# Performance work log

Measured on AMD Instinct MI355X. Metric: run time of the kernel, lower is better.

The kernel has to match this reference:

```python
import jax, jax.numpy as jnp
import numpy as np

EPS = 1e-12  # torch F.normalize eps


def unfold(x, ksize, pad):
    # torch F.unfold equivalent: [B,C,H,W] -> [B, C*k*k, L], channel-major ordering
    patches = jax.lax.conv_general_dilated_patches(
        x, (ksize, ksize), (1, 1), [(pad, pad), (pad, pad)],
        dimension_numbers=('NCHW', 'OIHW', 'NCHW'))
    B, CKK, Hp, Wp = patches.shape
    return patches.reshape(B, CKK, Hp * Wp)


def fold(patches, C, ksize, H, W, pad):
    # torch F.fold equivalent (stride 1): overlap-add of [B, C*k*k, H*W] -> [B,C,H,W]
    B = patches.shape[0]
    p = patches.reshape(B, C, ksize, ksize, H, W)
    out = jnp.zeros((B, C, H + 2 * pad, W + 2 * pad), patches.dtype)
    for di in range(ksize):
        for dj in range(ksize):
            out = out.at[:, :, di:di + H, dj:dj + W].add(p[:, :, di, dj])
    return out[:, :, pad:pad + H, pad:pad + W]


def setup_inputs() -> dict:
    key = jax.random.key(0)
    ks = jax.random.split(key, 4)
    B, C, H, W = 2, 512, 64, 64
    D, CIN = 256, 512 * 9  # embed: Linear(tdim*8*3*3 -> tdim*4), tdim=64
    return {
        'query': jax.random.normal(ks[0], (B, C, H, W), dtype=jnp.float32),
        'key': jax.random.normal(ks[1], (B, C, H, W), dtype=jnp.float32),
        'value': jax.random.normal(ks[2], (B, C, H, W), dtype=jnp.float32),
        'W_embed': jax.random.normal(ks[3], (D, CIN), dtype=jnp.float32) * 0.02,
        'k': 3,
    }


def reference(query, key, value, W_embed, k):
    B, Cv, H, W = value.shape
    # patch embed: unfold -> linear (no bias)
    q_unf = unfold(query, k, k // 2)                       # [B, C*k*k, L]
    k_unf = unfold(key, k, k // 2)                         # [B, C*k*k, L]
    k_emb = jnp.einsum('bcl,dc->bld', k_unf, W_embed)      # [B, L, D]
    q_emb = jnp.einsum('bcl,dc->bdl', q_unf, W_embed)      # [B, D, L]
    # cosine correlation
    k_n = k_emb / jnp.maximum(jnp.linalg.norm(k_emb, axis=2, keepdims=True), EPS)
    q_n = q_emb / jnp.maximum(jnp.linalg.norm(q_emb, axis=1, keepdims=True), EPS)
    corr = jnp.einsum('bld,bdm->blm', k_n, q_n)            # [B, L_key, L_query]
    corr_value = jnp.max(corr, axis=1)                     # [B, L]
    corr_argmax = jnp.argmax(corr, axis=1)                 # [B, L]
    # swap(V=value, idx=corr_argmax, s=1, k=k)
    s = 1
    temph = s * k + H * s - H - s                          # = k - 1
    tempw = s * k + W * s - W - s
    ph = max(temph // 2 + temph % 2, 1)
    pw = max(tempw // 2 + tempw % 2, 1)
    v_unf = unfold(value, k, ph)                           # [B, Cv*k*k, L] (ph==pw for square)
    t_unf = jnp.take_along_axis(v_unf, corr_argmax[:, None, :], axis=2)
    divisor = fold(jnp.ones_like(t_unf), Cv, k, H, W, ph)
    T = fold(t_unf, Cv, k, H, W, ph) / divisor             # [B, Cv, H, W]
    S = corr_value.reshape(B, 1, H, W)
    return S, T
```

## Files before the change

### kernel.cpp

```cpp
#include <hip/hip_runtime.h>
#include <hip/hip_bf16.h>
#include <stdint.h>
#include <math.h>

#define BB 2
#define CC 512
#define HH 64
#define WW 64
#define LL 4096
#define DD 256
#define CIN 4608
#define NG 144

typedef _Float16 half_t;
typedef __attribute__((ext_vector_type(8))) _Float16 f16x8;
typedef __attribute__((ext_vector_type(4))) _Float16 f16x4;
typedef __attribute__((ext_vector_type(4))) float f32x4;

__global__ __launch_bounds__(256) void presplit(const float* __restrict__ query,
                                                const float* __restrict__ key,
                                                char* __restrict__ img_ts) {
    __shared__ float tile[32][65];
    int img = blockIdx.y;
    int y   = blockIdx.x;
    const float* src = ((img >> 1) ? key : query) + (size_t)(img & 1) * CC * LL + y * WW;
    char* dstbase = img_ts + ((size_t)img * 64 + y) * (16 * 64 * 128);
    int t = threadIdx.x;
    int xl = t & 63, c4 = t >> 6;
    int xw = t >> 2, fsw = t & 3;
    for (int cc = 0; cc < 16; ++cc) {
#pragma unroll
        for (int j = 0; j < 8; ++j) {
            int cl = c4 + j * 4;
            tile[cl][xl] = src[(size_t)(cc * 32 + cl) * LL + xl];
        }
        __syncthreads();
        f16x8 h8, l8;
#pragma unroll
        for (int j = 0; j < 8; ++j) {
            float v = tile[fsw * 8 + j][xw];
            half_t h = (half_t)v;
            h8[j] = h; l8[j] = (half_t)(v - (float)h);
        }
        char* p = dstbase + (size_t)cc * 8192 + xw * 128;
        int swz = (xw & 7) << 4;
        *(f16x8*)(p + ((fsw * 16) ^ swz)) = h8;
        *(f16x8*)(p + ((64 + fsw * 16) ^ swz)) = l8;
        __syncthreads();
    }
}

__global__ __launch_bounds__(256) void splitW2b(const float* __restrict__ W,
                                                char* __restrict__ Wst) {
    int i = blockIdx.x * 256 + threadIdx.x;
    if (i >= NG * DD * 4) return;
    int g  = i >> 10;
    int r  = i & 1023;
    int d  = r >> 2;
    int fs = r & 3;
    int cc = g / 9, o = g - cc * 9;
    const float* src = W + (size_t)d * CIN;
    f16x8 h8, l8;
#pragma unroll
    for (int j = 0; j < 8; j++) {
        float w = src[(cc * 32 + fs * 8 + j) * 9 + o];
        half_t h = (half_t)w;
        h8[j] = h;
        l8[j] = (half_t)(w - (float)h);
    }
    size_t base = (size_t)g * 32768 + d * 128;
    int sw = (d & 7) << 4;
    *(f16x8*)(Wst + base + ((fs * 16) ^ sw)) = h8;
    *(f16x8*)(Wst + base + ((64 + fs * 16) ^ sw)) = l8;
}

#define GATE() do { asm volatile("s_waitcnt vmcnt(0) lgkmcnt(0)" ::: "memory"); \
                    __builtin_amdgcn_s_barrier(); \
                    __builtin_amdgcn_sched_barrier(0); } while (0)

__global__ __launch_bounds__(512, 1) void embed_mfma(const char* __restrict__ img_ts,
                                                     const char* __restrict__ Wst,
                                                     const char* __restrict__ zp,
                                                     float* __restrict__ part) {
    __shared__ char sW[2][32768];
    __shared__ char sB[2][33792];

    int iid = blockIdx.y;
    int ks  = blockIdx.z;
    int lt  = blockIdx.x;
    int y0  = lt * 2;
    int t = threadIdx.x;
    int w = t >> 6, lane = t & 63;
    int wr = w >> 1, wc = w & 1;
    int fr = lane & 15, fs = lane >> 4;

    const char* imgb = img_ts + (size_t)iid * (64 * 16 * 64 * 128) + (size_t)ks * 65536;
    const char *ps0, *ps1, *ps2, *ps3, *ps4;
    int pb0, pb1, pb2, pb3, pb4;
#define PREP(qv, PS, PB)                                                \
    {                                                                   \
        int q = (qv);                                                   \
        int ri = q / 528;                                               \
        int rem = q - ri * 528;                                         \
        int xi = rem >> 3, sub = rem & 7;                               \
        int xg = xi - 1, yg = y0 - 1 + ri;                              \
        bool ok = (yg >= 0) && (yg < 64) && (xg >= 0) && (xg < 64);     \
        PS = ok ? imgb + (size_t)yg * 131072 + (size_t)xg * 128 + sub * 16 \
                : zp + ((q & 255) * 16);                                \
        PB = ok ? 8192 : 0;                                             \
    }
    PREP(t, ps0, pb0); PREP(512 + t, ps1, pb1); PREP(1024 + t, ps2, pb2);
    PREP(1536 + t, ps3, pb3); PREP(2048 + t, ps4, pb4);

    const char* pW = Wst + (size_t)ks * 72 * 32768;

#define GLL(src, dst)                                                   \
    __builtin_amdgcn_global_load_lds(                                   \
        (const __attribute__((address_space(1))) void*)(src),           \
        (__attribute__((address_space(3))) void*)(dst), 16, 0, 0)

#define DMAW(dst)                                                       \
    do {                                                                \
        _Pragma("unroll")                                               \
        for (int c = 0; c < 4; c++)                                     \
            GLL(pW + c * 8192 + t * 16, (dst) + c * 8192 + t * 16);     \
        pW += 32768;                                                    \
    } while (0)

#define DMAB(dst)                                                       \
    do {                                                                \
        GLL(ps0, (dst) + t * 16);                                       \
        GLL(ps1, (dst) + 8192 + t * 16);                                \
        GLL(ps2, (dst) + 16384 + t * 16);                               \
        GLL(ps3, (dst) + 24576 + t * 16);                               \
        if (t < 64) GLL(ps4, (dst) + 32768 + t * 16);                   \
        ps0 += pb0; ps1 += pb1; ps2 += pb2; ps3 += pb3; ps4 += pb4;     \
    } while (0)

#define READA(wbuf)                                                     \
    do {                                                                \
        _Pragma("unroll")                                               \
        for (int rg = 0; rg < 4; rg++) {                                \
            int dl = wr * 64 + rg * 16 + fr;                            \
            int sw_ = (dl & 7) << 4;                                    \
            const char* rowp = (const char*)(wbuf) + dl * 128;          \
            ah[rg] = *(const f16x8*)(rowp + ((fs * 16) ^ sw_));         \
            al[rg] = *(const f16x8*)(rowp + ((64 + fs * 16) ^ sw_));    \
        }                                                               \
    } while (0)

#define READB(bbuf, di_, dj_)                                           \
    do {                                                                \
        int ri = wc + (di_);                                            \
        _Pragma("unroll")                                               \
        for (int cg = 0; cg < 4; cg++) {                                \
            int xi = cg * 16 + fr + (dj_);                              \
            int sw_ = ((xi - 1) & 7) << 4;                              \
            const char* rowp = (const char*)(bbuf) + ri * 8448 + xi * 128; \
            bh[cg] = *(const f16x8*)(rowp + ((fs * 16) ^ sw_));         \
            bl[cg] = *(const f16x8*)(rowp + ((64 + fs * 16) ^ sw_));    \
        }                                                               \
    } while (0)

#define DOMFMA()                                                        \
    do {                                                                \
        _Pragma("unroll")                                               \
        for (int rg = 0; rg < 4; rg++)                                  \
            _Pragma("unroll")                                           \
            for (int cg = 0; cg < 4; cg++)                              \
                acc[rg][cg] = __builtin_amdgcn_mfma_f32_16x16x32_f16(ah[rg], bh[cg], acc[rg][cg], 0, 0, 0); \
        _Pragma("unroll")                                               \
        for (int rg = 0; rg < 4; rg++)                                  \
            _Pragma("unroll")                                           \
            for (int cg = 0; cg < 4; cg++) {                            \
                acc[rg][cg] = __builtin_amdgcn_mfma_f32_16x16x32_f16(ah[rg], bl[cg], acc[rg][cg], 0, 0, 0); \
                acc[rg][cg] = __builtin_amdgcn_mfma_f32_16x16x32_f16(al[rg], bh[cg], acc[rg][cg], 0, 0, 0); \
            }                                                           \
    } while (0)

    f32x4 acc[4][4];
#pragma unroll
    for (int rg = 0; rg < 4; rg++)
#pragma unroll
        for (int cg = 0; cg < 4; cg++) acc[rg][cg] = (f32x4){0.f, 0.f, 0.f, 0.f};

    f16x8 ah[4], al[4], bh[4], bl[4];

    char* wb0 = &sW[0][0]; char* wb1 = &sW[1][0];
    char* b0 = &sB[0][0];  char* b1 = &sB[1][0];

    DMAB(b0);
    DMAW(wb0);
    GATE();

    char* wcur = wb0; char* wnext = wb1;
    char* bcur = b0;  char* bnext = b1;
    int o = 0, ccl = 0;

#pragma unroll 1
    for (int g = 0; g < 72; ++g) {
        int di_ = (o >= 6) ? 2 : (o >= 3) ? 1 : 0;
        int dj_ = o - di_ * 3;
        READA(wcur);
        READB(bcur, di_, dj_);
        if (g < 71) DMAW(wnext);
        if (o == 8 && ccl < 7) DMAB(bnext);
        __builtin_amdgcn_sched_barrier(0);
        DOMFMA();
        GATE();
        { char* tp = wcur; wcur = wnext; wnext = tp; }
        if (o == 8) { char* tp = bcur; bcur = bnext; bnext = tp; o = 0; ccl++; }
        else o++;
    }

    float* pt = part + (((size_t)iid * 32 + lt) * 2 + ks) * 32768;
#pragma unroll
    for (int rg = 0; rg < 4; rg++)
#pragma unroll
        for (int cg = 0; cg < 4; cg++) {
            int l = wc * 64 + cg * 16 + fr;
            int d0 = wr * 64 + rg * 16 + fs * 4;
#pragma unroll
            for (int r = 0; r < 4; r++)
                pt[(d0 + r) * 128 + l] = acc[rg][cg][r];
        }
#undef PREP
#undef GLL
#undef DMAW
#undef DMAB
#undef READA
#undef READB
#undef DOMFMA
}

__global__ __launch_bounds__(256) void norm_split(const float* __restrict__ part,
                                                  char* __restrict__ qemb,
                                                  char* __restrict__ kemb) {
    __shared__ float sm[4][64];
    __shared__ float invn[64];
    __shared__ char stage[64][1040];

    int iid = blockIdx.y;
    int bx  = blockIdx.x;
    int lt  = bx >> 1, lh2 = bx & 1;
    const float* p0 = part + (((size_t)iid * 32 + lt) * 2 + 0) * 32768 + lh2 * 64;
    const float* p1 = p0 + 32768;
    int t = threadIdx.x;
    int ll = t & 63, dq = t >> 6;

    float sq = 0.f;
    for (int dd = 0; dd < 64; ++dd) {
        int d = dq * 64 + dd;
        float v = p0[d * 128 + ll] + p1[d * 128 + ll];
        sq += v * v;
    }
    sm[dq][ll] = sq;
    __syncthreads();
    if (t < 64) {
        float s = sm[0][t] + sm[1][t] + sm[2][t] + sm[3][t];
        invn[t] = 1.0f / fmaxf(sqrtf(s), 1e-12f);
    }
    __syncthreads();

    float sc = invn[ll];
    int swb = (ll & 7) << 4;
    for (int oc = 0; oc < 8; ++oc) {
        int d0 = dq * 64 + oc * 8;
        f16x8 h8, l8;
#pragma unroll
        for (int j = 0; j < 8; ++j) {
            int d = d0 + j;
            float v = (p0[d * 128 + ll] + p1[d * 128 + ll]) * sc;
            half_t h = (half_t)v;
            h8[j] = h;
            l8[j] = (half_t)(v - (float)h);
        }
        int itb = d0 >> 5;
        int fsc = (d0 >> 3) & 3;
        *(f16x8*)&stage[ll][itb * 128 + ((fsc * 16) ^ swb)] = h8;
        *(f16x8*)&stage[ll][itb * 128 + ((64 + fsc * 16) ^ swb)] = l8;
    }
    __syncthreads();

    int b = iid & 1, type = iid >> 1;
    char* e = (type ? kemb : qemb);
    int rr = t >> 2, c0 = t & 3;
    char* erow = e + ((size_t)b * LL + lt * 128 + lh2 * 64 + rr) * 1024;
    const char* srow = &stage[rr][0];
#pragma unroll
    for (int c = 0; c < 16; ++c) {
        int cj = c0 + c * 4;
        *(float4*)(erow + cj * 16) = *(const float4*)(srow + cj * 16);
    }
}

__global__ void init_packed(unsigned long long* p, int n) {
    int i = blockIdx.x * 256 + threadIdx.x;
    if (i < n) p[i] = 0ull;
}

__global__ __launch_bounds__(256, 2) void corr_max_mfma(const char* __restrict__ kemb,
                                                        const char* __restrict__ qemb,
                                                        unsigned long long* __restrict__ packed) {
    __shared__ char sA[2][16384];
    __shared__ char sBq[2][16384];

    int b  = blockIdx.z;
    int l0 = blockIdx.y * 128;
    int m0 = blockIdx.x * 128;
    int t  = threadIdx.x;
    int w = t >> 6, lane = t & 63;
    int wr = w >> 1, wc = w & 1;
    int fr = lane & 15, fs = lane >> 4;

    const char* Abase = kemb + ((size_t)b * LL + l0) * 1024;
    const char* Bbase = qemb + ((size_t)b * LL + m0) * 1024;

    f32x4 acc[4][4];
#pragma unroll
    for (int i = 0; i < 4; i++)
#pragma unroll
        for (int j = 0; j < 4; j++) acc[i][j] = (f32x4){0.f, 0.f, 0.f, 0.f};

#define DMA2(bufi, itv)                                                   \
    do {                                                                  \
        _Pragma("unroll")                                                 \
        for (int c = 0; c < 4; c++) {                                     \
            int idx = c * 4096 + t * 16;                                  \
            int row = idx >> 7, offb = idx & 127;                         \
            __builtin_amdgcn_global_load_lds(                             \
                (const __attribute__((address_space(1))) void*)(Abase + (size_t)row * 1024 + (itv) * 128 + offb), \
                (__attribute__((address_space(3))) void*)(&sA[bufi][idx]), 16, 0, 0); \
        }                                                                 \
        _Pragma("unroll")                                                 \
        for (int c = 0; c < 4; c++) {                                     \
            int idx = c * 4096 + t * 16;                                  \
            int row = idx >> 7, offb = idx & 127;                         \
            __builtin_amdgcn_global_load_lds(                             \
                (const __attribute__((address_space(1))) void*)(Bbase + (size_t)row * 1024 + (itv) * 128 + offb), \
                (__attribute__((address_space(3))) void*)(&sBq[bufi][idx]), 16, 0, 0); \
        }                                                                 \
    } while (0)

    DMA2(0, 0);

    f16x8 ah[4], al[4], bh[4], bl[4];
    for (int it = 0; it < 8; ++it) {
        asm volatile("s_waitcnt vmcnt(0) lgkmcnt(0)" ::: "memory");
        __builtin_amdgcn_s_barrier();
        __builtin_amdgcn_sched_barrier(0);
        if (it < 7) DMA2((it + 1) & 1, it + 1);
        __builtin_amdgcn_sched_barrier(0);
        const char* sa = sA[it & 1];
        const char* sb = sBq[it & 1];
#pragma unroll
        for (int rg = 0; rg < 4; rg++) {
            int r = wr * 64 + rg * 16 + fr;
            const char* rp = sa + r * 128;
            int sw_ = (r & 7) << 4;
            ah[rg] = *(const f16x8*)(rp + ((fs * 16) ^ sw_));
            al[rg] = *(const f16x8*)(rp + ((64 + fs * 16) ^ sw_));
        }
#pragma unroll
        for (int cg = 0; cg < 4; cg++) {
            int r = wc * 64 + cg * 16 + fr;
            const char* rp = sb + r * 128;
            int sw_ = (r & 7) << 4;
            bh[cg] = *(const f16x8*)(rp + ((fs * 16) ^ sw_));
            bl[cg] = *(const f16x8*)(rp + ((64 + fs * 16) ^ sw_));
        }
#pragma unroll
        for (int rg = 0; rg < 4; rg++)
#pragma unroll
            for (int cg = 0; cg < 4; cg++)
                acc[rg][cg] = __builtin_amdgcn_mfma_f32_16x16x32_f16(ah[rg], bh[cg], acc[rg][cg], 0, 0, 0);
#pragma unroll
        for (int rg = 0; rg < 4; rg++)
#pragma unroll
            for (int cg = 0; cg < 4; cg++) {
                acc[rg][cg] = __builtin_amdgcn_mfma_f32_16x16x32_f16(ah[rg], bl[cg], acc[rg][cg], 0, 0, 0);
                acc[rg][cg] = __builtin_amdgcn_mfma_f32_16x16x32_f16(al[rg], bh[cg], acc[rg][cg], 0, 0, 0);
            }
    }
#undef DMA2

#pragma unroll
    for (int cg = 0; cg < 4; cg++) {
        unsigned long long best = 0ull;
#pragma unroll
        for (int rg = 0; rg < 4; rg++) {
#pragma unroll
            for (int r = 0; r < 4; r++) {
                unsigned u = __float_as_uint(acc[rg][cg][r]);
                u = (u & 0x80000000u) ? ~u : (u | 0x80000000u);
                int l = l0 + wr * 64 + rg * 16 + fs * 4 + r;
                unsigned long long p = ((unsigned long long)u << 32) | (unsigned)(4095 - l);
                best = (p > best) ? p : best;
            }
        }
        unsigned long long oo;
        oo = __shfl_xor(best, 16); best = (oo > best) ? oo : best;
        oo = __shfl_xor(best, 32); best = (oo > best) ? oo : best;
        if (lane < 16)
            atomicMax(&packed[(size_t)b * LL + m0 + wc * 64 + cg * 16 + lane], best);
    }
}

__global__ void decode_packed(const unsigned long long* __restrict__ packed,
                              float* __restrict__ S_out, int* __restrict__ arg) {
    int i = blockIdx.x * 256 + threadIdx.x;
    if (i < BB * LL) {
        unsigned long long p = packed[i];
        unsigned u = (unsigned)(p >> 32);
        unsigned bits = (u & 0x80000000u) ? (u & 0x7FFFFFFFu) : ~u;
        S_out[i] = __uint_as_float(bits);
        arg[i] = 4095 - (int)(unsigned)(p & 0xFFFFFFFFull);
    }
}

__global__ __launch_bounds__(256) void transpose_mat(const float* __restrict__ src,
                                                     float* __restrict__ dst,
                                                     int R, int Cc) {
    __shared__ float tile[32][33];
    size_t boff = (size_t)blockIdx.z * R * Cc;
    int bx = blockIdx.x;
    int by = blockIdx.y;
    int tx = threadIdx.x & 31;
    int ty = threadIdx.x >> 5;
    const float* s = src + boff;
    float* d = dst + boff;
#pragma unroll
    for (int i = 0; i < 4; i++) {
        int r = by * 32 + ty + i * 8;
        int c = bx * 32 + tx;
        tile[ty + i * 8][tx] = s[(size_t)r * Cc + c];
    }
    __syncthreads();
#pragma unroll
    for (int i = 0; i < 4; i++) {
        int c = bx * 32 + ty + i * 8;
        int r = by * 32 + tx;
        d[(size_t)c * R + r] = tile[tx][ty + i * 8];
    }
}

__global__ __launch_bounds__(256) void gather_fold(const float* __restrict__ value_t,
                                                   const int* __restrict__ arg,
                                                   float* __restrict__ T_t) {
    int b = blockIdx.y;
    int pix = blockIdx.x;
    int y = pix >> 6, x = pix & 63;
    int t = threadIdx.x;
    float2 acc = make_float2(0.f, 0.f);
    int cnty = (y == 0 || y == HH - 1) ? 2 : 3;
    int cntx = (x == 0 || x == WW - 1) ? 2 : 3;
    const int* ab = arg + b * LL;
    const float* vb = value_t + (size_t)b * LL * CC;
#pragma unroll
    for (int di = 0; di < 3; di++) {
        int my = y + 1 - di;
        if (my < 0 || my >= HH) continue;
#pragma unroll
        for (int dj = 0; dj < 3; dj++) {
            int mx = x + 1 - dj;
            if (mx < 0 || mx >= WW) continue;
            int a = ab[my * WW + mx];
            int ay = a >> 6, ax = a & 63;
            int vy = ay + di - 1, vx = ax + dj - 1;
            if (vy < 0 || vy >= HH || vx < 0 || vx >= WW) continue;
            float2 v = *(const float2*)&vb[((size_t)(vy * WW + vx)) * CC + t * 2];
            acc.x += v.x; acc.y += v.y;
        }
    }
    float inv = 1.0f / (float)(cnty * cntx);
    acc.x *= inv; acc.y *= inv;
    *(float2*)&T_t[((size_t)b * LL + pix) * CC + t * 2] = acc;
}

extern "C" void kernel_launch(void* const* d_in, const int* in_sizes, int n_in,
                              void* d_out, int out_size, void* d_ws, size_t ws_size,
                              hipStream_t stream) {
    const float* query = (const float*)d_in[0];
    const float* key   = (const float*)d_in[1];
    const float* value = (const float*)d_in[2];
    const float* Wemb  = (const float*)d_in[3];

    float* out   = (float*)d_out;
    float* S_out = out;
    float* T_out = out + BB * LL;

    char* ws = (char*)d_ws;
    char*  img_ts = ws;
    char*  Wst    = ws + 33554432;
    float* part   = (float*)(ws + 38273024);
    char*  qemb   = ws + 71827456;
    char*  kemb   = ws + 80216064;
    unsigned long long* packed = (unsigned long long*)(ws + 88604672);
    char*  zp     = ws + 88670208;
    int*   arg    = (int*)(ws + 88674304);
    float* val_t  = (float*)(ws + 38273024);
    float* T_t    = (float*)(ws + 38273024 + 16777216);

    init_packed   <<<dim3(34), 256, 0, stream>>>(packed, 8704);
    presplit      <<<dim3(64, 4), 256, 0, stream>>>(query, key, img_ts);
    splitW2b      <<<dim3(576), 256, 0, stream>>>(Wemb, Wst);
    embed_mfma    <<<dim3(32, 4, 2), 512, 0, stream>>>(img_ts, Wst, zp, part);
    norm_split    <<<dim3(64, 4), 256, 0, stream>>>(part, qemb, kemb);
    corr_max_mfma <<<dim3(32, 32, 2), 256, 0, stream>>>(kemb, qemb, packed);
    decode_packed <<<dim3(32), 256, 0, stream>>>(packed, S_out, arg);
    transpose_mat <<<dim3(128, 16, 2), 256, 0, stream>>>(value, val_t, CC, LL);
    gather_fold   <<<dim3(4096, 2), 256, 0, stream>>>(val_t, arg, T_t);
    transpose_mat <<<dim3(16, 128, 2), 256, 0, stream>>>(T_t, T_out, LL, CC);
}
```

Baseline: 221.7 us.

## Restructure embed GEMM pipeline with unrolled double-buffered A loads and 8x1 wave tiling

Reworks the embed MFMA kernel. Each wave now owns 32 output rows across all 128 columns instead of a 4x2 wave grid. The 72-step loop is fully unrolled into 18-step bodies with precomputed LDS pointers, and weight fragments for the next step are prefetched into alternating register sets. The wait-all plus barrier gate is replaced with partial vmcnt waits and a barrier only at image-tile boundaries, so global loads overlap compute. Launch bounds request two blocks per CU, which limits registers, and norm_split caches values in registers so the partial-sum buffer is not read twice. Fewer barriers raise the risk of LDS race conditions if the vmcnt accounting is wrong.

```diff
diff --git a/kernel.cpp b/kernel.cpp
--- a/kernel.cpp
+++ b/kernel.cpp
@@ -74,11 +74,7 @@
     *(f16x8*)(Wst + base + ((64 + fs * 16) ^ sw)) = l8;
 }
 
-#define GATE() do { asm volatile("s_waitcnt vmcnt(0) lgkmcnt(0)" ::: "memory"); \
-                    __builtin_amdgcn_s_barrier(); \
-                    __builtin_amdgcn_sched_barrier(0); } while (0)
-
-__global__ __launch_bounds__(512, 1) void embed_mfma(const char* __restrict__ img_ts,
+__global__ __launch_bounds__(512, 2) void embed_mfma(const char* __restrict__ img_ts,
                                                      const char* __restrict__ Wst,
                                                      const char* __restrict__ zp,
                                                      float* __restrict__ part) {
@@ -91,7 +87,6 @@
     int y0  = lt * 2;
     int t = threadIdx.x;
     int w = t >> 6, lane = t & 63;
-    int wr = w >> 1, wc = w & 1;
     int fr = lane & 15, fs = lane >> 4;
 
     const char* imgb = img_ts + (size_t)iid * (64 * 16 * 64 * 128) + (size_t)ks * 65536;
@@ -112,114 +107,137 @@
     PREP(t, ps0, pb0); PREP(512 + t, ps1, pb1); PREP(1024 + t, ps2, pb2);
     PREP(1536 + t, ps3, pb3); PREP(2048 + t, ps4, pb4);
 
-    const char* pW = Wst + (size_t)ks * 72 * 32768;
+    const char* pWl = Wst + (size_t)ks * 72 * 32768 + (w << 12) + lane * 16;
+    char* wdst0 = &sW[0][0] + (w << 12) + lane * 16;
+    char* wdst1 = wdst0 + 32768;
+    char* bB0 = &sB[0][0] + t * 16;
+
+    int swzA = (fr & 7) << 4;
+    const char* aBH = &sW[0][0] + (w << 12) + fr * 128 + ((fs * 16) ^ swzA);
+    const char* aBL = &sW[0][0] + (w << 12) + fr * 128 + ((64 + fs * 16) ^ swzA);
+    const char* bH0 = &sB[0][0] + (fr + 0) * 128 + ((fs * 16) ^ (((fr - 1) & 7) << 4));
+    const char* bL0 = &sB[0][0] + (fr + 0) * 128 + (((64 + fs * 16)) ^ (((fr - 1) & 7) << 4));
+    const char* bH1 = &sB[0][0] + (fr + 1) * 128 + ((fs * 16) ^ (((fr) & 7) << 4));
+    const char* bL1 = &sB[0][0] + (fr + 1) * 128 + (((64 + fs * 16)) ^ (((fr) & 7) << 4));
+    const char* bH2 = &sB[0][0] + (fr + 2) * 128 + ((fs * 16) ^ (((fr + 1) & 7) << 4));
+    const char* bL2 = &sB[0][0] + (fr + 2) * 128 + (((64 + fs * 16)) ^ (((fr + 1) & 7) << 4));
 
 #define GLL(src, dst)                                                   \
     __builtin_amdgcn_global_load_lds(                                   \
         (const __attribute__((address_space(1))) void*)(src),           \
         (__attribute__((address_space(3))) void*)(dst), 16, 0, 0)
 
-#define DMAW(dst)                                                       \
+#define DMAW(SEL)                                                       \
+    do {                                                                \
+        char* wd_ = (SEL) ? wdst1 : wdst0;                              \
+        GLL(pWl, wd_);                                                  \
+        GLL(pWl + 1024, wd_ + 1024);                                    \
+        GLL(pWl + 2048, wd_ + 2048);                                    \
+        GLL(pWl + 3072, wd_ + 3072);                                    \
+        pWl += 32768;                                                   \
+    } while (0)
+
+#define DMAB(SEL)                                                       \
+    do {                                                                \
+        char* bd_ = bB0 + (SEL) * 33792;                                \
+        GLL(ps0, bd_);                                                  \
+        GLL(ps1, bd_ + 8192);                                           \
+        GLL(ps2, bd_ + 16384);                                          \
+        GLL(ps3, bd_ + 24576);                                          \
+        if (t < 64) GLL(ps4, bd_ + 32768);                              \
+        ps0 += pb0; ps1 += pb1; ps2 += pb2; ps3 += pb3; ps4 += pb4;     \
+    } while (0)
+
+#define RDA(AH, AL, BSEL)                                               \
+    do {                                                                \
+        AH[0] = *(const f16x8*)(aBH + (BSEL) * 32768);                  \
+        AL[0] = *(const f16x8*)(aBL + (BSEL) * 32768);                  \
+        AH[1] = *(const f16x8*)(aBH + 2048 + (BSEL) * 32768);           \
+        AL[1] = *(const f16x8*)(aBL + 2048 + (BSEL) * 32768);           \
+    } while (0)
+
+#define RDB(DI, DJ, CSEL)                                               \
+    do {                                                                \
+        const char* h_ = (DJ) == 0 ? bH0 : (DJ) == 1 ? bH1 : bH2;       \
+        const char* l_ = (DJ) == 0 ? bL0 : (DJ) == 1 ? bL1 : bL2;       \
+        _Pragma("unroll")                                               \
+        for (int cg = 0; cg < 8; cg++) {                                \
+            int imm = ((cg >> 2) + (DI)) * 8448 + (cg & 3) * 2048 + (CSEL) * 33792; \
+            bh[cg] = *(const f16x8*)(h_ + imm);                         \
+            bl[cg] = *(const f16x8*)(l_ + imm);                         \
+        }                                                               \
+    } while (0)
+
+#define DOMFMA(AH, AL)                                                  \
     do {                                                                \
         _Pragma("unroll")                                               \
-        for (int c = 0; c < 4; c++)                                     \
-            GLL(pW + c * 8192 + t * 16, (dst) + c * 8192 + t * 16);     \
-        pW += 32768;                                                    \
-    } while (0)
-
-#define DMAB(dst)                                                       \
+        for (int rg = 0; rg < 2; rg++)                                  \
+            _Pragma("unroll")                                           \
+            for (int cg = 0; cg < 8; cg++)                              \
+                acc[rg][cg] = __builtin_amdgcn_mfma_f32_16x16x32_f16(AH[rg], bh[cg], acc[rg][cg], 0, 0, 0); \
+        _Pragma("unroll")                                               \
+        for (int rg = 0; rg < 2; rg++)                                  \
+            _Pragma("unroll")                                           \
+            for (int cg = 0; cg < 8; cg++) {                            \
+                acc[rg][cg] = __builtin_amdgcn_mfma_f32_16x16x32_f16(AH[rg], bl[cg], acc[rg][cg], 0, 0, 0); \
+                acc[rg][cg] = __builtin_amdgcn_mfma_f32_16x16x32_f16(AL[rg], bh[cg], acc[rg][cg], 0, 0, 0); \
+            }                                                           \
+    } while (0)
+
+    f32x4 acc[2][8];
+#pragma unroll
+    for (int rg = 0; rg < 2; rg++)
+#pragma unroll
+        for (int cg = 0; cg < 8; cg++) acc[rg][cg] = (f32x4){0.f, 0.f, 0.f, 0.f};
+
+    f16x8 ah0[2], al0[2], ah1[2], al1[2];
+    f16x8 bh[8], bl[8];
+
+    DMAB(0);
+    DMAW(0);
+    DMAW(1);
+    asm volatile("s_waitcnt vmcnt(4)" ::: "memory");
+    __builtin_amdgcn_sched_barrier(0);
+    RDA(ah0, al0, 0);
+    __builtin_amdgcn_sched_barrier(0);
+
+#define BODY(KK, O, CSEL, NSEL, DI, DJ)                                 \
     do {                                                                \
-        GLL(ps0, (dst) + t * 16);                                       \
-        GLL(ps1, (dst) + 8192 + t * 16);                                \
-        GLL(ps2, (dst) + 16384 + t * 16);                               \
-        GLL(ps3, (dst) + 24576 + t * 16);                               \
-        if (t < 64) GLL(ps4, (dst) + 32768 + t * 16);                   \
-        ps0 += pb0; ps1 += pb1; ps2 += pb2; ps3 += pb3; ps4 += pb4;     \
-    } while (0)
-
-#define READA(wbuf)                                                     \
-    do {                                                                \
-        _Pragma("unroll")                                               \
-        for (int rg = 0; rg < 4; rg++) {                                \
-            int dl = wr * 64 + rg * 16 + fr;                            \
-            int sw_ = (dl & 7) << 4;                                    \
-            const char* rowp = (const char*)(wbuf) + dl * 128;          \
-            ah[rg] = *(const f16x8*)(rowp + ((fs * 16) ^ sw_));         \
-            al[rg] = *(const f16x8*)(rowp + ((64 + fs * 16) ^ sw_));    \
-        }                                                               \
-    } while (0)
-
-#define READB(bbuf, di_, dj_)                                           \
-    do {                                                                \
-        int ri = wc + (di_);                                            \
-        _Pragma("unroll")                                               \
-        for (int cg = 0; cg < 4; cg++) {                                \
-            int xi = cg * 16 + fr + (dj_);                              \
-            int sw_ = ((xi - 1) & 7) << 4;                              \
-            const char* rowp = (const char*)(bbuf) + ri * 8448 + xi * 128; \
-            bh[cg] = *(const f16x8*)(rowp + ((fs * 16) ^ sw_));         \
-            bl[cg] = *(const f16x8*)(rowp + ((64 + fs * 16) ^ sw_));    \
-        }                                                               \
-    } while (0)
-
-#define DOMFMA()                                                        \
-    do {                                                                \
-        _Pragma("unroll")                                               \
-        for (int rg = 0; rg < 4; rg++)                                  \
-            _Pragma("unroll")                                           \
-            for (int cg = 0; cg < 4; cg++)                              \
-                acc[rg][cg] = __builtin_amdgcn_mfma_f32_16x16x32_f16(ah[rg], bh[cg], acc[rg][cg], 0, 0, 0); \
-        _Pragma("unroll")                                               \
-        for (int rg = 0; rg < 4; rg++)                                  \
-            _Pragma("unroll")                                           \
-            for (int cg = 0; cg < 4; cg++) {                            \
-                acc[rg][cg] = __builtin_amdgcn_mfma_f32_16x16x32_f16(ah[rg], bl[cg], acc[rg][cg], 0, 0, 0); \
-                acc[rg][cg] = __builtin_amdgcn_mfma_f32_16x16x32_f16(al[rg], bh[cg], acc[rg][cg], 0, 0, 0); \
-            }                                                           \
-    } while (0)
-
-    f32x4 acc[4][4];
-#pragma unroll
-    for (int rg = 0; rg < 4; rg++)
-#pragma unroll
-        for (int cg = 0; cg < 4; cg++) acc[rg][cg] = (f32x4){0.f, 0.f, 0.f, 0.f};
-
-    f16x8 ah[4], al[4], bh[4], bl[4];
-
-    char* wb0 = &sW[0][0]; char* wb1 = &sW[1][0];
-    char* b0 = &sB[0][0];  char* b1 = &sB[1][0];
-
-    DMAB(b0);
-    DMAW(wb0);
-    GATE();
-
-    char* wcur = wb0; char* wnext = wb1;
-    char* bcur = b0;  char* bnext = b1;
-    int o = 0, ccl = 0;
+        if ((O) == 0) __builtin_amdgcn_s_barrier();                     \
+        asm volatile("s_waitcnt lgkmcnt(0)" ::: "memory");              \
+        __builtin_amdgcn_sched_barrier(0);                              \
+        DMAW((KK) & 1);                                                 \
+        if ((O) == 1) DMAB(NSEL);                                       \
+        if ((O) == 1 || (O) == 2)                                       \
+            asm volatile("s_waitcnt vmcnt(8)" ::: "memory");            \
+        else                                                            \
+            asm volatile("s_waitcnt vmcnt(4)" ::: "memory");            \
+        __builtin_amdgcn_sched_barrier(0);                              \
+        if ((KK) & 1) { RDA(ah0, al0, ((KK) + 1) & 1); }                \
+        else          { RDA(ah1, al1, ((KK) + 1) & 1); }                \
+        RDB(DI, DJ, CSEL);                                              \
+        __builtin_amdgcn_sched_barrier(0);                              \
+        if ((KK) & 1) DOMFMA(ah1, al1); else DOMFMA(ah0, al0);          \
+    } while (0)
 
 #pragma unroll 1
-    for (int g = 0; g < 72; ++g) {
-        int di_ = (o >= 6) ? 2 : (o >= 3) ? 1 : 0;
-        int dj_ = o - di_ * 3;
-        READA(wcur);
-        READB(bcur, di_, dj_);
-        if (g < 71) DMAW(wnext);
-        if (o == 8 && ccl < 7) DMAB(bnext);
-        __builtin_amdgcn_sched_barrier(0);
-        DOMFMA();
-        GATE();
-        { char* tp = wcur; wcur = wnext; wnext = tp; }
-        if (o == 8) { char* tp = bcur; bcur = bnext; bnext = tp; o = 0; ccl++; }
-        else o++;
-    }
+    for (int cp = 0; cp < 4; ++cp) {
+        BODY(0, 0, 0, 1, 0, 0);  BODY(1, 1, 0, 1, 0, 1);  BODY(2, 2, 0, 1, 0, 2);
+        BODY(3, 3, 0, 1, 1, 0);  BODY(4, 4, 0, 1, 1, 1);  BODY(5, 5, 0, 1, 1, 2);
+        BODY(6, 6, 0, 1, 2, 0);  BODY(7, 7, 0, 1, 2, 1);  BODY(8, 8, 0, 1, 2, 2);
+        BODY(9, 0, 1, 0, 0, 0);  BODY(10, 1, 1, 0, 0, 1); BODY(11, 2, 1, 0, 0, 2);
+        BODY(12, 3, 1, 0, 1, 0); BODY(13, 4, 1, 0, 1, 1); BODY(14, 5, 1, 0, 1, 2);
+        BODY(15, 6, 1, 0, 2, 0); BODY(16, 7, 1, 0, 2, 1); BODY(17, 8, 1, 0, 2, 2);
+    }
+#undef BODY
 
     float* pt = part + (((size_t)iid * 32 + lt) * 2 + ks) * 32768;
 #pragma unroll
-    for (int rg = 0; rg < 4; rg++)
-#pragma unroll
-        for (int cg = 0; cg < 4; cg++) {
-            int l = wc * 64 + cg * 16 + fr;
-            int d0 = wr * 64 + rg * 16 + fs * 4;
+    for (int rg = 0; rg < 2; rg++)
+#pragma unroll
+        for (int cg = 0; cg < 8; cg++) {
+            int l = cg * 16 + fr;
+            int d0 = w * 32 + rg * 16 + fs * 4;
 #pragma unroll
             for (int r = 0; r < 4; r++)
                 pt[(d0 + r) * 128 + l] = acc[rg][cg][r];
@@ -228,8 +246,8 @@
 #undef GLL
 #undef DMAW
 #undef DMAB
-#undef READA
-#undef READB
+#undef RDA
+#undef RDB
 #undef DOMFMA
 }
 
@@ -248,11 +266,14 @@
     int t = threadIdx.x;
     int ll = t & 63, dq = t >> 6;
 
+    float v[64];
     float sq = 0.f;
+#pragma unroll
     for (int dd = 0; dd < 64; ++dd) {
         int d = dq * 64 + dd;
-        float v = p0[d * 128 + ll] + p1[d * 128 + ll];
-        sq += v * v;
+        float x = p0[d * 128 + ll] + p1[d * 128 + ll];
+        v[dd] = x;
+        sq += x * x;
     }
     sm[dq][ll] = sq;
     __syncthreads();
@@ -264,16 +285,16 @@
 
     float sc = invn[ll];
     int swb = (ll & 7) << 4;
+#pragma unroll
     for (int oc = 0; oc < 8; ++oc) {
         int d0 = dq * 64 + oc * 8;
         f16x8 h8, l8;
 #pragma unroll
         for (int j = 0; j < 8; ++j) {
-            int d = d0 + j;
-            float v = (p0[d * 128 + ll] + p1[d * 128 + ll]) * sc;
-            half_t h = (half_t)v;
+            float x = v[oc * 8 + j] * sc;
+            half_t h = (half_t)x;
             h8[j] = h;
-            l8[j] = (half_t)(v - (float)h);
+            l8[j] = (half_t)(x - (float)h);
         }
         int itb = d0 >> 5;
         int fsc = (d0 >> 3) & 3;
```

Result: faster. 208.5 us (median of 2 runs) (-5.9%).
